# Kernel tuning notes

Hardware: AMD Instinct MI355X
Metric: run time of the kernel (lower is better)

Reference implementation:

```python
import jax, jax.numpy as jnp
import numpy as np

N, E, DIN, H, EIN, EH, STEPS = 10000, 100000, 64, 64, 16, 128, 3


def setup_inputs() -> dict:
    key = jax.random.key(0)
    ks = jax.random.split(key, 8)
    n_feat = jax.random.normal(ks[0], (N, DIN), jnp.float32)
    e_feat = jax.random.normal(ks[1], (E, EIN), jnp.float32)
    src = jax.random.randint(ks[2], (E,), 0, N, jnp.int32)
    dst = jax.random.randint(ks[3], (E,), 0, N, jnp.int32)
    W0 = jax.random.normal(ks[4], (DIN, H), jnp.float32) / np.sqrt(DIN)
    b0 = jnp.zeros((H,), jnp.float32)
    We1 = jax.random.normal(ks[5], (EIN, EH), jnp.float32) / np.sqrt(EIN)
    be1 = jnp.zeros((EH,), jnp.float32)
    # small scale so per-edge HxH weight matrices keep activations stable
    We2 = jax.random.normal(ks[6], (EH, H * H), jnp.float32) * 0.02
    be2 = jnp.zeros((H * H,), jnp.float32)
    conv_bias = jnp.zeros((H,), jnp.float32)
    gamma = jnp.ones((H,), jnp.float32)
    beta = jnp.zeros((H,), jnp.float32)
    return {"n_feat": n_feat, "e_feat": e_feat, "src": src, "dst": dst,
            "W0": W0, "b0": b0, "We1": We1, "be1": be1, "We2": We2,
            "be2": be2, "conv_bias": conv_bias, "gamma": gamma, "beta": beta}


def reference(n_feat, e_feat, src, dst, W0, b0, We1, be1, We2, be2, conv_bias, gamma, beta):
    n = n_feat.shape[0]
    h = W0.shape[1]
    out = jax.nn.relu(n_feat @ W0 + b0)  # [N,H]
    # edge network (eval mode: dropout = identity); e_feat is fixed so the
    # per-edge weight matrices are identical each step -> compute once.
    w_edge = (jax.nn.relu(e_feat @ We1 + be1) @ We2 + be2).reshape(-1, h, h)  # [E,H,H]
    for _ in range(STEPS):
        msg = jnp.einsum('ei,eio->eo', out[src], w_edge)  # gather + per-edge matmul
        agg = jax.ops.segment_sum(msg, dst, num_segments=n)  # scatter-sum to dst
        out = jax.nn.relu(agg + conv_bias)
    # BatchNorm1d over nodes (training-mode batch statistics)
    mean = jnp.mean(out, axis=0)
    var = jnp.var(out, axis=0)
    return (out - mean) * jax.lax.rsqrt(var + 1e-5) * gamma + beta
```

## Files before the change

### kernel.cpp

```cpp
#include <hip/hip_runtime.h>
#include <stdint.h>

#define DIN   64
#define HDIM  64
#define EIN   16
#define EHID  128
#define HH    4096
#define TC    8256
#define STEPS 3

typedef short bf16x8 __attribute__((ext_vector_type(8)));
typedef float f32x4  __attribute__((ext_vector_type(4)));

__device__ __forceinline__ unsigned short f32_to_bf16(float f) {
    union { float f; uint32_t u; } v; v.f = f;
    uint32_t r = v.u + 0x7fffu + ((v.u >> 16) & 1u);
    return (unsigned short)(r >> 16);
}
__device__ __forceinline__ float bfu_to_f(unsigned short u) {
    union { uint32_t u; float f; } v; v.u = (uint32_t)u << 16; return v.f;
}

__global__ void k_pro(const float* __restrict__ nf, const float* __restrict__ W0,
                      const float* __restrict__ b0, float* __restrict__ outb,
                      unsigned short* __restrict__ outbf,
                      const float* __restrict__ ef, const float* __restrict__ We1,
                      const float* __restrict__ be1, unsigned short* __restrict__ h,
                      const float* __restrict__ We2, const float* __restrict__ be2,
                      unsigned short* __restrict__ BmatT,
                      const int* __restrict__ src, const int* __restrict__ dst,
                      int* __restrict__ cntS, int* __restrict__ cntD,
                      int n_nodes, int n_edges, int nbN, int nbE, int nbB) {
    __shared__ float smem[DIN * HDIM];
    int b = blockIdx.x, tid = threadIdx.x;
    if (b < nbN) {
        for (int i = tid; i < DIN * HDIM; i += 256) smem[i] = W0[i];
        __syncthreads();
        int node = b * 4 + (tid >> 6);
        int o = tid & 63;
        if (node >= n_nodes) return;
        float xr = nf[node * DIN + o];
        float acc = b0[o];
#pragma unroll 8
        for (int i = 0; i < DIN; ++i)
            acc += __shfl(xr, i, 64) * smem[i * HDIM + o];
        float v = fmaxf(acc, 0.f);
        outb[node * HDIM + o] = v;
        outbf[node * HDIM + o] = f32_to_bf16(v);
    } else if (b < nbN + nbE) {
        int wave = tid >> 6, lane = tid & 63;
        int r = lane & 15, q = lane >> 4;
        int e0 = (b - nbN) * 64 + wave * 16;
        if (e0 >= n_edges) return;
        bf16x8 afr = (bf16x8){};
        bf16x8 bfr[8];
#pragma unroll
        for (int nt = 0; nt < 8; ++nt) bfr[nt] = (bf16x8){};
        if (q < 2) {
            int ea = e0 + r; if (ea >= n_edges) ea = n_edges - 1;
            const float* xa = ef + (size_t)ea * EIN + q * 8;
#pragma unroll
            for (int j = 0; j < 8; ++j) afr[j] = (short)f32_to_bf16(xa[j]);
#pragma unroll
            for (int nt = 0; nt < 8; ++nt)
#pragma unroll
                for (int j = 0; j < 8; ++j)
                    bfr[nt][j] = (short)f32_to_bf16(We1[(q * 8 + j) * EHID + nt * 16 + r]);
        }
        f32x4 acc[8];
#pragma unroll
        for (int nt = 0; nt < 8; ++nt)
            acc[nt] = __builtin_amdgcn_mfma_f32_16x16x32_bf16(afr, bfr[nt], (f32x4){}, 0, 0, 0);
        float bias[8];
#pragma unroll
        for (int nt = 0; nt < 8; ++nt) bias[nt] = be1[nt * 16 + r];
#pragma unroll
        for (int rg = 0; rg < 4; ++rg) {
            int e = e0 + q * 4 + rg;
            if (e >= n_edges) continue;
            ushort4 pk0, pk1;
            pk0.x = f32_to_bf16(fmaxf(acc[0][rg] + bias[0], 0.f));
            pk0.y = f32_to_bf16(fmaxf(acc[1][rg] + bias[1], 0.f));
            pk0.z = f32_to_bf16(fmaxf(acc[2][rg] + bias[2], 0.f));
            pk0.w = f32_to_bf16(fmaxf(acc[3][rg] + bias[3], 0.f));
            pk1.x = f32_to_bf16(fmaxf(acc[4][rg] + bias[4], 0.f));
            pk1.y = f32_to_bf16(fmaxf(acc[5][rg] + bias[5], 0.f));
            pk1.z = f32_to_bf16(fmaxf(acc[6][rg] + bias[6], 0.f));
            pk1.w = f32_to_bf16(fmaxf(acc[7][rg] + bias[7], 0.f));
            *(ushort4*)(h + (size_t)e * EHID + 4 * r) = pk0;
            *(ushort4*)(h + (size_t)e * EHID + 64 + 4 * r) = pk1;
        }
    } else if (b < nbN + nbE + nbB) {
        int t = (b - nbN - nbE) * 256 + tid;
        if (t >= TC * 64) return;
        int c = t >> 6, i = t & 63;
        int m;
        if (c < 8192) {
            int g = c & 127;
            m = (c & ~127) + 8 * (g & 15) + (g >> 4);
        } else {
            int g = c & 63;
            m = (c & ~63) + 4 * (g & 15) + (g >> 4);
        }
        float v;
        if (m < 8192) {
            int p = ((m >> 11) << 5) | (m & 31);
            int k = (p & 64) + ((p & 3) << 4) + ((p >> 2) & 15);
            int o = (m >> 5) & 63;
            v = We2[k * HH + i * 64 + o];
        } else {
            v = be2[i * 64 + (m - 8192)];
        }
        BmatT[t] = f32_to_bf16(v);
    } else {
        int e = (b - nbN - nbE - nbB) * 256 + tid;
        if (e >= n_edges) return;
        atomicAdd(&cntS[src[e]], 1);
        atomicAdd(&cntD[dst[e]], 1);
    }
}

__global__ void k_T(const unsigned short* __restrict__ outbf, const unsigned short* __restrict__ BmatT,
                    unsigned short* __restrict__ T, int n0, int n1) {
    int wave = threadIdx.x >> 6, lane = threadIdx.x & 63;
    int r = lane & 15, q = lane >> 4;
    int eb = n0 + blockIdx.y * 128;
    if (blockIdx.x < 16) {
        int cb = blockIdx.x * 512 + wave * 128;
        bf16x8 bfr[8][2];
#pragma unroll
        for (int nt = 0; nt < 8; ++nt) {
            size_t cofs = (size_t)(cb + nt * 16 + r) * 64;
            bfr[nt][0] = *(const bf16x8*)(BmatT + cofs + q * 8);
            bfr[nt][1] = *(const bf16x8*)(BmatT + cofs + 32 + q * 8);
        }
#pragma unroll
        for (int mt = 0; mt < 8; ++mt) {
            int e = eb + mt * 16 + r;
            if (e >= n1) e = n1 - 1;
            bf16x8 afr0 = *(const bf16x8*)(outbf + (size_t)e * 64 + q * 8);
            bf16x8 afr1 = *(const bf16x8*)(outbf + (size_t)e * 64 + 32 + q * 8);
            f32x4 acc[8];
#pragma unroll
            for (int nt = 0; nt < 8; ++nt) {
                acc[nt] = __builtin_amdgcn_mfma_f32_16x16x32_bf16(afr0, bfr[nt][0], (f32x4){}, 0, 0, 0);
                acc[nt] = __builtin_amdgcn_mfma_f32_16x16x32_bf16(afr1, bfr[nt][1], acc[nt], 0, 0, 0);
            }
#pragma unroll
            for (int rg = 0; rg < 4; ++rg) {
                int n = eb + mt * 16 + q * 4 + rg;
                if (n >= n1) continue;
                ushort4 pa, pb;
                pa.x = f32_to_bf16(acc[0][rg]); pa.y = f32_to_bf16(acc[1][rg]);
                pa.z = f32_to_bf16(acc[2][rg]); pa.w = f32_to_bf16(acc[3][rg]);
                pb.x = f32_to_bf16(acc[4][rg]); pb.y = f32_to_bf16(acc[5][rg]);
                pb.z = f32_to_bf16(acc[6][rg]); pb.w = f32_to_bf16(acc[7][rg]);
                uint4 pk = { ((uint32_t)pa.y << 16) | pa.x, ((uint32_t)pa.w << 16) | pa.z,
                             ((uint32_t)pb.y << 16) | pb.x, ((uint32_t)pb.w << 16) | pb.z };
                *(uint4*)(T + (size_t)(n - n0) * TC + cb + 8 * r) = pk;
            }
        }
    } else {
        if (wave != 0) return;
        int cb = 8192;
        bf16x8 bfr[4][2];
#pragma unroll
        for (int nt = 0; nt < 4; ++nt) {
            size_t cofs = (size_t)(cb + nt * 16 + r) * 64;
            bfr[nt][0] = *(const bf16x8*)(BmatT + cofs + q * 8);
            bfr[nt][1] = *(const bf16x8*)(BmatT + cofs + 32 + q * 8);
        }
#pragma unroll
        for (int mt = 0; mt < 8; ++mt) {
            int e = eb + mt * 16 + r;
            if (e >= n1) e = n1 - 1;
            bf16x8 afr0 = *(const bf16x8*)(outbf + (size_t)e * 64 + q * 8);
            bf16x8 afr1 = *(const bf16x8*)(outbf + (size_t)e * 64 + 32 + q * 8);
            f32x4 acc[4];
#pragma unroll
            for (int nt = 0; nt < 4; ++nt) {
                acc[nt] = __builtin_amdgcn_mfma_f32_16x16x32_bf16(afr0, bfr[nt][0], (f32x4){}, 0, 0, 0);
                acc[nt] = __builtin_amdgcn_mfma_f32_16x16x32_bf16(afr1, bfr[nt][1], acc[nt], 0, 0, 0);
            }
#pragma unroll
            for (int rg = 0; rg < 4; ++rg) {
                int n = eb + mt * 16 + q * 4 + rg;
                if (n >= n1) continue;
                ushort4 pk;
                pk.x = f32_to_bf16(acc[0][rg]);
                pk.y = f32_to_bf16(acc[1][rg]);
                pk.z = f32_to_bf16(acc[2][rg]);
                pk.w = f32_to_bf16(acc[3][rg]);
                *(ushort4*)(T + (size_t)(n - n0) * TC + cb + 4 * r) = pk;
            }
        }
    }
}

__global__ void k_msg(const unsigned short* __restrict__ h, const unsigned short* __restrict__ T,
                      const int* __restrict__ offS, const int* __restrict__ permS,
                      float* __restrict__ msg, int n0, int n1) {
    int wave = threadIdx.x >> 6, lane = threadIdx.x & 63;
    int n = n0 + blockIdx.x * 4 + wave;
    if (n >= n1) return;
    int beg = offS[n], end = offS[n + 1];
    if (beg == end) return;
    int r = lane & 15, q = lane >> 4;
    const unsigned short* Tb = T + (size_t)(n - n0) * TC;
    float bias[4];
#pragma unroll
    for (int nt = 0; nt < 4; ++nt)
        bias[nt] = bfu_to_f(Tb[8192 + nt * 16 + r]);
    for (int j0 = beg; j0 < end; j0 += 16) {
        int jc = j0 + r; if (jc >= end) jc = end - 1;
        int e = permS[jc];
        const unsigned short* he = h + (size_t)e * EHID;
        f32x4 acc[4] = {};
#pragma unroll
        for (int s = 0; s < 4; ++s) {
            bf16x8 afr = *(const bf16x8*)(he + s * 32 + q * 8);
#pragma unroll
            for (int nt = 0; nt < 4; ++nt) {
                bf16x8 bfr = *(const bf16x8*)(Tb + s * 2048 + (nt * 16 + r) * 32 + q * 8);
                acc[nt] = __builtin_amdgcn_mfma_f32_16x16x32_bf16(afr, bfr, acc[nt], 0, 0, 0);
            }
        }
#pragma unroll
        for (int rg = 0; rg < 4; ++rg) {
            int jr = j0 + q * 4 + rg;
            if (jr >= end) continue;
            int er = permS[jr];
            f32x4 pk = { acc[0][rg] + bias[0], acc[1][rg] + bias[1],
                         acc[2][rg] + bias[2], acc[3][rg] + bias[3] };
            *(f32x4*)(msg + (size_t)er * 64 + 4 * r) = pk;
        }
    }
}

__global__ void k_scan(const int* __restrict__ cntS, const int* __restrict__ cntD,
                       int* __restrict__ offS, int* __restrict__ offD,
                       int* __restrict__ curS, int* __restrict__ curD, int n, int total) {
    const int* cnt = blockIdx.x ? cntD : cntS;
    int* off = blockIdx.x ? offD : offS;
    int* cur = blockIdx.x ? curD : curS;
    __shared__ int part[256];
    int tid = threadIdx.x;
    int chunk = (n + 255) / 256;
    int c0 = tid * chunk, c1 = c0 + chunk; if (c1 > n) c1 = n; if (c0 > n) c0 = n;
    int s = 0;
    for (int i = c0; i < c1; ++i) s += cnt[i];
    part[tid] = s;
    __syncthreads();
    for (int st = 1; st < 256; st <<= 1) {
        int v = (tid >= st) ? part[tid - st] : 0;
        __syncthreads();
        part[tid] += v;
        __syncthreads();
    }
    int run = tid ? part[tid - 1] : 0;
    for (int i = c0; i < c1; ++i) { off[i] = run; cur[i] = run; run += cnt[i]; }
    if (tid == 0) off[n] = total;
}

__global__ void k_perm(const int* __restrict__ src, const int* __restrict__ dst,
                       int* __restrict__ curS, int* __restrict__ curD,
                       int* __restrict__ permS, int* __restrict__ permD, int n_edges) {
    int e = blockIdx.x * 256 + threadIdx.x;
    if (e >= n_edges) return;
    permS[atomicAdd(&curS[src[e]], 1)] = e;
    permD[atomicAdd(&curD[dst[e]], 1)] = e;
}

__global__ void k_agg(const float* __restrict__ msg, const int* __restrict__ offD,
                      const int* __restrict__ permD, const float* __restrict__ cbias,
                      float* __restrict__ outb, unsigned short* __restrict__ outbf, int n_nodes) {
    int wave = threadIdx.x >> 6, lane = threadIdx.x & 63;
    int d = blockIdx.x * 4 + wave;
    if (d >= n_nodes) return;
    int o = (lane & 3) * 16 + (lane >> 2);
    float acc = 0.f;
    int end = offD[d + 1];
    for (int j = offD[d]; j < end; ++j)
        acc += msg[(size_t)permD[j] * 64 + lane];
    float v = fmaxf(acc + cbias[o], 0.f);
    outb[(size_t)d * 64 + o] = v;
    outbf[(size_t)d * 64 + o] = f32_to_bf16(v);
}

__global__ void k_bn_stats(const float* __restrict__ out, float* __restrict__ stat, int n_nodes) {
    __shared__ float s1[256], s2[256];
    int tid = threadIdx.x;
    int f = tid & 63, g = tid >> 6;
    float sum = 0.f, ss = 0.f;
    for (int r = blockIdx.x * 4 + g; r < n_nodes; r += 256) {
        float v = out[r * HDIM + f];
        sum += v; ss += v * v;
    }
    s1[tid] = sum; s2[tid] = ss;
    __syncthreads();
    if (tid < 64) {
        float A = s1[tid] + s1[64 + tid] + s1[128 + tid] + s1[192 + tid];
        float B = s2[tid] + s2[64 + tid] + s2[128 + tid] + s2[192 + tid];
        atomicAdd(&stat[tid], A);
        atomicAdd(&stat[64 + tid], B);
    }
}

__global__ void k_bn_apply(const float* __restrict__ out, const float* __restrict__ stat,
                           const float* __restrict__ gamma, const float* __restrict__ beta,
                           float* __restrict__ y, int n, int n_nodes) {
    int t = blockIdx.x * 256 + threadIdx.x;
    if (t >= n) return;
    int f = t & 63;
    float mean = stat[f] / n_nodes;
    float var  = stat[64 + f] / n_nodes - mean * mean;
    float inv  = rsqrtf(var + 1e-5f);
    float scale = gamma[f] * inv;
    float shift = beta[f] - mean * scale;
    y[t] = out[t] * scale + shift;
}

extern "C" void kernel_launch(void* const* d_in, const int* in_sizes, int n_in,
                              void* d_out, int out_size, void* d_ws, size_t ws_size,
                              hipStream_t stream) {
    const float* nf    = (const float*)d_in[0];
    const float* ef    = (const float*)d_in[1];
    const int*   src   = (const int*)d_in[2];
    const int*   dst   = (const int*)d_in[3];
    const float* W0    = (const float*)d_in[4];
    const float* b0    = (const float*)d_in[5];
    const float* We1   = (const float*)d_in[6];
    const float* be1   = (const float*)d_in[7];
    const float* We2   = (const float*)d_in[8];
    const float* be2   = (const float*)d_in[9];
    const float* cbias = (const float*)d_in[10];
    const float* gamma = (const float*)d_in[11];
    const float* beta  = (const float*)d_in[12];
    (void)n_in; (void)out_size;

    int n_nodes = in_sizes[0] / DIN;
    int n_edges = in_sizes[2];

    char* ws = (char*)d_ws;
    size_t off = 0;
    auto carve = [&](size_t bytes) -> void* {
        void* p = ws + off;
        off = (off + bytes + 255) & ~(size_t)255;
        return p;
    };
    unsigned short* h     = (unsigned short*)carve((size_t)n_edges * EHID * 2);
    float*          msg   = (float*)carve((size_t)n_edges * 64 * 4);
    float*          outb  = (float*)carve((size_t)n_nodes * HDIM * 4);
    unsigned short* outbf = (unsigned short*)carve((size_t)n_nodes * HDIM * 2);
    unsigned short* BmatT = (unsigned short*)carve((size_t)TC * 64 * 2);
    int*            offS  = (int*)carve((size_t)(n_nodes + 1) * 4);
    int*            offD  = (int*)carve((size_t)(n_nodes + 1) * 4);
    int*            curS  = (int*)carve((size_t)n_nodes * 4);
    int*            curD  = (int*)carve((size_t)n_nodes * 4);
    int*            permS = (int*)carve((size_t)n_edges * 4);
    int*            permD = (int*)carve((size_t)n_edges * 4);
    float*          stat  = (float*)carve(128 * 4 + (size_t)2 * n_nodes * 4);
    int*            cntS  = (int*)(stat + 128);
    int*            cntD  = cntS + n_nodes;
    unsigned short* T     = (unsigned short*)(ws + off);
    size_t avail = ws_size > off ? ws_size - off : 0;
    long tcap = (long)(avail / ((size_t)TC * 2));
    if (tcap > n_nodes) tcap = n_nodes;
    if (tcap < 64) tcap = 64;
    long tchunk = tcap;

    hipMemsetAsync(stat, 0, 128 * 4 + (size_t)2 * n_nodes * 4, stream);

    int nbN = (n_nodes + 3) / 4;
    int nbE = (n_edges + 63) / 64;
    int nbB = (TC * 64 + 255) / 256;
    int nbH = (n_edges + 255) / 256;
    k_pro<<<dim3(nbN + nbE + nbB + nbH), 256, 0, stream>>>(
        nf, W0, b0, outb, outbf, ef, We1, be1, h, We2, be2, BmatT,
        src, dst, cntS, cntD, n_nodes, n_edges, nbN, nbE, nbB);
    k_scan<<<dim3(2), 256, 0, stream>>>(cntS, cntD, offS, offD, curS, curD, n_nodes, n_edges);
    k_perm<<<dim3((n_edges + 255) / 256), 256, 0, stream>>>(src, dst, curS, curD, permS, permD, n_edges);

    for (int step = 0; step < STEPS; ++step) {
        for (long n0 = 0; n0 < n_nodes; n0 += tchunk) {
            long n1 = n0 + tchunk; if (n1 > n_nodes) n1 = n_nodes;
            long cnt = n1 - n0;
            k_T<<<dim3(17, (cnt + 127) / 128), 256, 0, stream>>>(
                outbf, BmatT, T, (int)n0, (int)n1);
            k_msg<<<dim3((cnt + 3) / 4), 256, 0, stream>>>(
                h, T, offS, permS, msg, (int)n0, (int)n1);
        }
        k_agg<<<dim3((n_nodes + 3) / 4), 256, 0, stream>>>(msg, offD, permD, cbias, outb, outbf, n_nodes);
    }

    k_bn_stats<<<dim3(64), 256, 0, stream>>>(outb, stat, n_nodes);
    k_bn_apply<<<dim3((n_nodes * HDIM + 255) / 256), 256, 0, stream>>>(
        outb, stat, gamma, beta, (float*)d_out, n_nodes * HDIM, n_nodes);
}
```

Before: 427.8 us.

## Replace CSR gather aggregation with atomic scatter-add fused into message kernel

The message kernel now atomically adds each per-edge message straight into a per-step aggregation buffer indexed by dst. This removes the fp32 msg buffer, the dst permutation and CSR build, and the separate k_agg pass. The bias+ReLU of the aggregate is applied lazily in the next step's k_T and in the batchnorm kernels, and feature order is permuted to match the MFMA output layout. In exchange it issues many global float atomics, which can contend and make the sums nondeterministic, and it needs a larger memset to zero three aggregation buffers.

```diff
diff --git a/kernel.cpp b/kernel.cpp
--- a/kernel.cpp
+++ b/kernel.cpp
@@ -12,6 +12,7 @@
 typedef short bf16x8 __attribute__((ext_vector_type(8)));
 typedef float f32x4  __attribute__((ext_vector_type(4)));
 
+
 __device__ __forceinline__ unsigned short f32_to_bf16(float f) {
     union { float f; uint32_t u; } v; v.f = f;
     uint32_t r = v.u + 0x7fffu + ((v.u >> 16) & 1u);
@@ -22,12 +23,12 @@
 }
 
 __global__ void k_pro(const float* __restrict__ nf, const float* __restrict__ W0,
-                      const float* __restrict__ b0, float* __restrict__ outb,
-                      unsigned short* __restrict__ outbf,
+                      const float* __restrict__ b0, unsigned short* __restrict__ outbf,
                       const float* __restrict__ ef, const float* __restrict__ We1,
                       const float* __restrict__ be1, unsigned short* __restrict__ h,
                       const float* __restrict__ We2, const float* __restrict__ be2,
                       unsigned short* __restrict__ BmatT,
+                      const float* __restrict__ cbias, float* __restrict__ cbp,
                       const int* __restrict__ src, const int* __restrict__ dst,
                       int* __restrict__ cntS, int* __restrict__ cntD,
                       int n_nodes, int n_edges, int nbN, int nbE, int nbB) {
@@ -45,8 +46,8 @@
         for (int i = 0; i < DIN; ++i)
             acc += __shfl(xr, i, 64) * smem[i * HDIM + o];
         float v = fmaxf(acc, 0.f);
-        outb[node * HDIM + o] = v;
-        outbf[node * HDIM + o] = f32_to_bf16(v);
+        int p = ((o & 15) << 2) | (o >> 4);
+        outbf[node * HDIM + p] = f32_to_bf16(v);
     } else if (b < nbN + nbE) {
         int wave = tid >> 6, lane = tid & 63;
         int r = lane & 15, q = lane >> 4;
@@ -92,8 +93,11 @@
         }
     } else if (b < nbN + nbE + nbB) {
         int t = (b - nbN - nbE) * 256 + tid;
+        if (b == nbN + nbE && tid < 64)
+            cbp[tid] = cbias[(tid & 3) * 16 + (tid >> 2)];
         if (t >= TC * 64) return;
         int c = t >> 6, i = t & 63;
+        int isem = (i & 3) * 16 + (i >> 2);
         int m;
         if (c < 8192) {
             int g = c & 127;
@@ -107,9 +111,9 @@
             int p = ((m >> 11) << 5) | (m & 31);
             int k = (p & 64) + ((p & 3) << 4) + ((p >> 2) & 15);
             int o = (m >> 5) & 63;
-            v = We2[k * HH + i * 64 + o];
+            v = We2[k * HH + isem * 64 + o];
         } else {
-            v = be2[i * 64 + (m - 8192)];
+            v = be2[isem * 64 + (m - 8192)];
         }
         BmatT[t] = f32_to_bf16(v);
     } else {
@@ -120,17 +124,23 @@
     }
 }
 
-__global__ void k_T(const unsigned short* __restrict__ outbf, const unsigned short* __restrict__ BmatT,
+__global__ void k_T(const unsigned short* __restrict__ outbf, const float* __restrict__ aggp,
+                    const float* __restrict__ cbp, const unsigned short* __restrict__ BmatT,
                     unsigned short* __restrict__ T, int n0, int n1) {
     int wave = threadIdx.x >> 6, lane = threadIdx.x & 63;
     int r = lane & 15, q = lane >> 4;
     int eb = n0 + blockIdx.y * 128;
+    float cb[16];
+    if (aggp) {
+#pragma unroll
+        for (int j = 0; j < 8; ++j) { cb[j] = cbp[q * 8 + j]; cb[8 + j] = cbp[32 + q * 8 + j]; }
+    }
     if (blockIdx.x < 16) {
-        int cb = blockIdx.x * 512 + wave * 128;
+        int cbase = blockIdx.x * 512 + wave * 128;
         bf16x8 bfr[8][2];
 #pragma unroll
         for (int nt = 0; nt < 8; ++nt) {
-            size_t cofs = (size_t)(cb + nt * 16 + r) * 64;
+            size_t cofs = (size_t)(cbase + nt * 16 + r) * 64;
             bfr[nt][0] = *(const bf16x8*)(BmatT + cofs + q * 8);
             bfr[nt][1] = *(const bf16x8*)(BmatT + cofs + 32 + q * 8);
         }
@@ -138,8 +148,18 @@
         for (int mt = 0; mt < 8; ++mt) {
             int e = eb + mt * 16 + r;
             if (e >= n1) e = n1 - 1;
-            bf16x8 afr0 = *(const bf16x8*)(outbf + (size_t)e * 64 + q * 8);
-            bf16x8 afr1 = *(const bf16x8*)(outbf + (size_t)e * 64 + 32 + q * 8);
+            bf16x8 afr0, afr1;
+            if (aggp) {
+                const float* ap = aggp + (size_t)e * 64 + q * 8;
+#pragma unroll
+                for (int j = 0; j < 8; ++j) {
+                    afr0[j] = (short)f32_to_bf16(fmaxf(ap[j] + cb[j], 0.f));
+                    afr1[j] = (short)f32_to_bf16(fmaxf(ap[32 + j] + cb[8 + j], 0.f));
+                }
+            } else {
+                afr0 = *(const bf16x8*)(outbf + (size_t)e * 64 + q * 8);
+                afr1 = *(const bf16x8*)(outbf + (size_t)e * 64 + 32 + q * 8);
+            }
             f32x4 acc[8];
 #pragma unroll
             for (int nt = 0; nt < 8; ++nt) {
@@ -157,16 +177,16 @@
                 pb.z = f32_to_bf16(acc[6][rg]); pb.w = f32_to_bf16(acc[7][rg]);
                 uint4 pk = { ((uint32_t)pa.y << 16) | pa.x, ((uint32_t)pa.w << 16) | pa.z,
                              ((uint32_t)pb.y << 16) | pb.x, ((uint32_t)pb.w << 16) | pb.z };
-                *(uint4*)(T + (size_t)(n - n0) * TC + cb + 8 * r) = pk;
+                *(uint4*)(T + (size_t)(n - n0) * TC + cbase + 8 * r) = pk;
             }
         }
     } else {
         if (wave != 0) return;
-        int cb = 8192;
+        int cbase = 8192;
         bf16x8 bfr[4][2];
 #pragma unroll
         for (int nt = 0; nt < 4; ++nt) {
-            size_t cofs = (size_t)(cb + nt * 16 + r) * 64;
+            size_t cofs = (size_t)(cbase + nt * 16 + r) * 64;
             bfr[nt][0] = *(const bf16x8*)(BmatT + cofs + q * 8);
             bfr[nt][1] = *(const bf16x8*)(BmatT + cofs + 32 + q * 8);
         }
@@ -174,8 +194,18 @@
         for (int mt = 0; mt < 8; ++mt) {
             int e = eb + mt * 16 + r;
             if (e >= n1) e = n1 - 1;
-            bf16x8 afr0 = *(const bf16x8*)(outbf + (size_t)e * 64 + q * 8);
-            bf16x8 afr1 = *(const bf16x8*)(outbf + (size_t)e * 64 + 32 + q * 8);
+            bf16x8 afr0, afr1;
+            if (aggp) {
+                const float* ap = aggp + (size_t)e * 64 + q * 8;
+#pragma unroll
+                for (int j = 0; j < 8; ++j) {
+                    afr0[j] = (short)f32_to_bf16(fmaxf(ap[j] + cb[j], 0.f));
+                    afr1[j] = (short)f32_to_bf16(fmaxf(ap[32 + j] + cb[8 + j], 0.f));
+                }
+            } else {
+                afr0 = *(const bf16x8*)(outbf + (size_t)e * 64 + q * 8);
+                afr1 = *(const bf16x8*)(outbf + (size_t)e * 64 + 32 + q * 8);
+            }
             f32x4 acc[4];
 #pragma unroll
             for (int nt = 0; nt < 4; ++nt) {
@@ -191,7 +221,7 @@
                 pk.y = f32_to_bf16(acc[1][rg]);
                 pk.z = f32_to_bf16(acc[2][rg]);
                 pk.w = f32_to_bf16(acc[3][rg]);
-                *(ushort4*)(T + (size_t)(n - n0) * TC + cb + 4 * r) = pk;
+                *(ushort4*)(T + (size_t)(n - n0) * TC + cbase + 4 * r) = pk;
             }
         }
     }
@@ -199,7 +229,7 @@
 
 __global__ void k_msg(const unsigned short* __restrict__ h, const unsigned short* __restrict__ T,
                       const int* __restrict__ offS, const int* __restrict__ permS,
-                      float* __restrict__ msg, int n0, int n1) {
+                      const int* __restrict__ dst, float* __restrict__ agg, int n0, int n1) {
     int wave = threadIdx.x >> 6, lane = threadIdx.x & 63;
     int n = n0 + blockIdx.x * 4 + wave;
     if (n >= n1) return;
@@ -230,9 +260,11 @@
             int jr = j0 + q * 4 + rg;
             if (jr >= end) continue;
             int er = permS[jr];
-            f32x4 pk = { acc[0][rg] + bias[0], acc[1][rg] + bias[1],
-                         acc[2][rg] + bias[2], acc[3][rg] + bias[3] };
-            *(f32x4*)(msg + (size_t)er * 64 + 4 * r) = pk;
+            float* ag = agg + (size_t)dst[er] * 64 + 4 * r;
+            atomicAdd(ag + 0, acc[0][rg] + bias[0]);
+            atomicAdd(ag + 1, acc[1][rg] + bias[1]);
+            atomicAdd(ag + 2, acc[2][rg] + bias[2]);
+            atomicAdd(ag + 3, acc[3][rg] + bias[3]);
         }
     }
 }
@@ -262,38 +294,22 @@
     if (tid == 0) off[n] = total;
 }
 
-__global__ void k_perm(const int* __restrict__ src, const int* __restrict__ dst,
-                       int* __restrict__ curS, int* __restrict__ curD,
-                       int* __restrict__ permS, int* __restrict__ permD, int n_edges) {
+__global__ void k_perm(const int* __restrict__ src,
+                       int* __restrict__ curS, int* __restrict__ permS, int n_edges) {
     int e = blockIdx.x * 256 + threadIdx.x;
     if (e >= n_edges) return;
     permS[atomicAdd(&curS[src[e]], 1)] = e;
-    permD[atomicAdd(&curD[dst[e]], 1)] = e;
-}
-
-__global__ void k_agg(const float* __restrict__ msg, const int* __restrict__ offD,
-                      const int* __restrict__ permD, const float* __restrict__ cbias,
-                      float* __restrict__ outb, unsigned short* __restrict__ outbf, int n_nodes) {
-    int wave = threadIdx.x >> 6, lane = threadIdx.x & 63;
-    int d = blockIdx.x * 4 + wave;
-    if (d >= n_nodes) return;
-    int o = (lane & 3) * 16 + (lane >> 2);
-    float acc = 0.f;
-    int end = offD[d + 1];
-    for (int j = offD[d]; j < end; ++j)
-        acc += msg[(size_t)permD[j] * 64 + lane];
-    float v = fmaxf(acc + cbias[o], 0.f);
-    outb[(size_t)d * 64 + o] = v;
-    outbf[(size_t)d * 64 + o] = f32_to_bf16(v);
-}
-
-__global__ void k_bn_stats(const float* __restrict__ out, float* __restrict__ stat, int n_nodes) {
+}
+
+__global__ void k_bn_stats(const float* __restrict__ agg, const float* __restrict__ cbp,
+                           float* __restrict__ stat, int n_nodes) {
     __shared__ float s1[256], s2[256];
     int tid = threadIdx.x;
     int f = tid & 63, g = tid >> 6;
+    float cb = cbp[f];
     float sum = 0.f, ss = 0.f;
     for (int r = blockIdx.x * 4 + g; r < n_nodes; r += 256) {
-        float v = out[r * HDIM + f];
+        float v = fmaxf(agg[r * HDIM + f] + cb, 0.f);
         sum += v; ss += v * v;
     }
     s1[tid] = sum; s2[tid] = ss;
@@ -306,18 +322,21 @@
     }
 }
 
-__global__ void k_bn_apply(const float* __restrict__ out, const float* __restrict__ stat,
+__global__ void k_bn_apply(const float* __restrict__ agg, const float* __restrict__ cbp,
+                           const float* __restrict__ stat,
                            const float* __restrict__ gamma, const float* __restrict__ beta,
                            float* __restrict__ y, int n, int n_nodes) {
     int t = blockIdx.x * 256 + threadIdx.x;
     if (t >= n) return;
-    int f = t & 63;
-    float mean = stat[f] / n_nodes;
-    float var  = stat[64 + f] / n_nodes - mean * mean;
+    int l = t & 63;
+    int f = (l & 3) * 16 + (l >> 2);
+    float v = fmaxf(agg[t] + cbp[l], 0.f);
+    float mean = stat[l] / n_nodes;
+    float var  = stat[64 + l] / n_nodes - mean * mean;
     float inv  = rsqrtf(var + 1e-5f);
     float scale = gamma[f] * inv;
     float shift = beta[f] - mean * scale;
-    y[t] = out[t] * scale + shift;
+    y[(t & ~63) | f] = v * scale + shift;
 }
 
 extern "C" void kernel_launch(void* const* d_in, const int* in_sizes, int n_in,
@@ -349,51 +368,50 @@
         return p;
     };
     unsigned short* h     = (unsigned short*)carve((size_t)n_edges * EHID * 2);
-    float*          msg   = (float*)carve((size_t)n_edges * 64 * 4);
-    float*          outb  = (float*)carve((size_t)n_nodes * HDIM * 4);
     unsigned short* outbf = (unsigned short*)carve((size_t)n_nodes * HDIM * 2);
     unsigned short* BmatT = (unsigned short*)carve((size_t)TC * 64 * 2);
     int*            offS  = (int*)carve((size_t)(n_nodes + 1) * 4);
-    int*            offD  = (int*)carve((size_t)(n_nodes + 1) * 4);
     int*            curS  = (int*)carve((size_t)n_nodes * 4);
-    int*            curD  = (int*)carve((size_t)n_nodes * 4);
     int*            permS = (int*)carve((size_t)n_edges * 4);
-    int*            permD = (int*)carve((size_t)n_edges * 4);
-    float*          stat  = (float*)carve(128 * 4 + (size_t)2 * n_nodes * 4);
-    int*            cntS  = (int*)(stat + 128);
-    int*            cntD  = cntS + n_nodes;
-    unsigned short* T     = (unsigned short*)(ws + off);
+    float*          cbp   = (float*)carve(64 * 4);
+    size_t zbytes = 128 * 4 + (size_t)2 * n_nodes * 4 + (size_t)3 * n_nodes * HDIM * 4;
+    float* stat = (float*)carve(zbytes);
+    int*   cntS = (int*)(stat + 128);
+    int*   cntD = cntS + n_nodes;
+    float* agg0 = (float*)(cntD + n_nodes);
+    float* agg[3] = { agg0, agg0 + (size_t)n_nodes * HDIM, agg0 + (size_t)2 * n_nodes * HDIM };
+    unsigned short* T = (unsigned short*)(ws + off);
     size_t avail = ws_size > off ? ws_size - off : 0;
     long tcap = (long)(avail / ((size_t)TC * 2));
     if (tcap > n_nodes) tcap = n_nodes;
     if (tcap < 64) tcap = 64;
     long tchunk = tcap;
 
-    hipMemsetAsync(stat, 0, 128 * 4 + (size_t)2 * n_nodes * 4, stream);
+    hipMemsetAsync(stat, 0, zbytes, stream);
 
     int nbN = (n_nodes + 3) / 4;
     int nbE = (n_edges + 63) / 64;
     int nbB = (TC * 64 + 255) / 256;
     int nbH = (n_edges + 255) / 256;
     k_pro<<<dim3(nbN + nbE + nbB + nbH), 256, 0, stream>>>(
-        nf, W0, b0, outb, outbf, ef, We1, be1, h, We2, be2, BmatT,
-        src, dst, cntS, cntD, n_nodes, n_edges, nbN, nbE, nbB);
-    k_scan<<<dim3(2), 256, 0, stream>>>(cntS, cntD, offS, offD, curS, curD, n_nodes, n_edges);
-    k_perm<<<dim3((n_edges + 255) / 256), 256, 0, stream>>>(src, dst, curS, curD, permS, permD, n_edges);
+        nf, W0, b0, outbf, ef, We1, be1, h, We2, be2, BmatT,
+        cbias, cbp, src, dst, cntS, cntD, n_nodes, n_edges, nbN, nbE, nbB);
+    k_scan<<<dim3(1), 256, 0, stream>>>(cntS, cntS, offS, offS, curS, curS, n_nodes, n_edges);
+    k_perm<<<dim3((n_edges + 255) / 256), 256, 0, stream>>>(src, curS, permS, n_edges);
 
     for (int step = 0; step < STEPS; ++step) {
+        const float* aggprev = (step == 0) ? nullptr : agg[step - 1];
         for (long n0 = 0; n0 < n_nodes; n0 += tchunk) {
             long n1 = n0 + tchunk; if (n1 > n_nodes) n1 = n_nodes;
             long cnt = n1 - n0;
             k_T<<<dim3(17, (cnt + 127) / 128), 256, 0, stream>>>(
-                outbf, BmatT, T, (int)n0, (int)n1);
+                outbf, aggprev, cbp, BmatT, T, (int)n0, (int)n1);
             k_msg<<<dim3((cnt + 3) / 4), 256, 0, stream>>>(
-                h, T, offS, permS, msg, (int)n0, (int)n1);
-        }
-        k_agg<<<dim3((n_nodes + 3) / 4), 256, 0, stream>>>(msg, offD, permD, cbias, outb, outbf, n_nodes);
-    }
-
-    k_bn_stats<<<dim3(64), 256, 0, stream>>>(outb, stat, n_nodes);
+                h, T, offS, permS, dst, agg[step], (int)n0, (int)n1);
+        }
+    }
+
+    k_bn_stats<<<dim3(64), 256, 0, stream>>>(agg[2], cbp, stat, n_nodes);
     k_bn_apply<<<dim3((n_nodes * HDIM + 255) / 256), 256, 0, stream>>>(
-        outb, stat, gamma, beta, (float*)d_out, n_nodes * HDIM, n_nodes);
-}
+        agg[2], cbp, stat, gamma, beta, (float*)d_out, n_nodes * HDIM, n_nodes);
+}
```

Result: slower. 565.3 us (+32.1%).
